# Optimization experiments

Measured on AMD Instinct MI355X. Metric: run time of the kernel, lower is better.

Reference implementation:

```python
import jax, jax.numpy as jnp
import numpy as np

N = 8192
IN_FEAT = 256
OUT_FEAT = 128
SLOPE = 0.1
NEG_INF = -9e15


def setup_inputs() -> dict:
    key = jax.random.key(0)
    k_doc, k_Ww, k_Wb, k_aw, k_ab = jax.random.split(key, 5)
    doc = jax.random.normal(k_doc, (N, IN_FEAT), dtype=jnp.float32)
    # nn.Linear(inFeat, outFeat): weight [out, in], bias [out]
    W_w = jax.random.normal(k_Ww, (OUT_FEAT, IN_FEAT), dtype=jnp.float32) / np.sqrt(IN_FEAT)
    W_b = jax.random.normal(k_Wb, (OUT_FEAT,), dtype=jnp.float32) * 0.01
    # nn.Linear(2*outFeat, 1): weight [1, 2*out], bias [1]
    a_w = jax.random.normal(k_aw, (1, 2 * OUT_FEAT), dtype=jnp.float32) / np.sqrt(2 * OUT_FEAT)
    a_b = jax.random.normal(k_ab, (1,), dtype=jnp.float32) * 0.01
    return {"doc": doc, "W_w": W_w, "W_b": W_b, "a_w": a_w, "a_b": a_b, "selfLink": 0}


def reference(doc, W_w, W_b, a_w, a_b, selfLink):
    # h = W(doc)  -> [N, outFeat]
    h = doc @ W_w.T + W_b
    n = h.shape[0]
    # Original builds fch[i, j] = concat(h_i, h_j) -> [N, N, 2D] and applies
    # Linear(2D, 1). Algebraically: score[i,j] = h_i . a_src + h_j . a_dst + b,
    # where a_src/a_dst are the two halves of the weight. Same math, O(N*D) mem.
    a_src = a_w[0, :OUT_FEAT]   # [D]
    a_dst = a_w[0, OUT_FEAT:]   # [D]
    s_src = h @ a_src           # [N]
    s_dst = h @ a_dst           # [N]
    att = jax.nn.leaky_relu(s_src[:, None] + s_dst[None, :] + a_b[0], SLOPE)  # [N, N]
    if selfLink == 0:
        # adj = 1 - eye: mask self-edges
        diag = jnp.eye(n, dtype=bool)
        att = jnp.where(diag, NEG_INF, att)
    att = jax.nn.softmax(att, axis=1)
    h_out = jax.nn.leaky_relu(att @ h, SLOPE)  # [N, D]
    return (h_out, att)
```

## Files before the change

### kernel.cpp

```cpp
#include <hip/hip_runtime.h>
#include <math.h>

#define NROW 8192
#define IN_F 256
#define OUT_F 128
#define SLOPE 0.1f

__device__ __forceinline__ float lrelu(float x) { return x > 0.f ? x : SLOPE * x; }

__global__ __launch_bounds__(256) void k1_h(const float* __restrict__ doc,
                                            const float* __restrict__ Ww,
                                            const float* __restrict__ Wb,
                                            float* __restrict__ h) {
    __shared__ float4 sdoc[16][64];
    const int t = threadIdx.x;
    const int rowBase = blockIdx.x * 16;
    const float4* doc4 = (const float4*)(doc + (size_t)rowBase * IN_F);
    float4* sflat = &sdoc[0][0];
    for (int i = t; i < 16 * 64; i += 256) sflat[i] = doc4[i];
    __syncthreads();
    const int c = t & 127;
    const int rg = t >> 7;
    float acc[8];
#pragma unroll
    for (int r = 0; r < 8; ++r) acc[r] = 0.f;
    const float4* w4 = (const float4*)(Ww + (size_t)c * IN_F);
    for (int k = 0; k < 64; ++k) {
        const float4 w = w4[k];
#pragma unroll
        for (int r = 0; r < 8; ++r) {
            const float4 d = sdoc[2 * r + rg][k];
            acc[r] += d.x * w.x + d.y * w.y + d.z * w.z + d.w * w.w;
        }
    }
    const float b = Wb[c];
#pragma unroll
    for (int r = 0; r < 8; ++r)
        h[(size_t)(rowBase + 2 * r + rg) * OUT_F + c] = acc[r] + b;
}

__global__ __launch_bounds__(256) void k1b_sv(const float* __restrict__ h,
                                              const float* __restrict__ aw,
                                              float* __restrict__ s_src,
                                              float* __restrict__ s_dst) {
    const int wave = threadIdx.x >> 6, lane = threadIdx.x & 63;
    const int row = blockIdx.x * 4 + wave;
    const float2 hv = ((const float2*)(h + (size_t)row * OUT_F))[lane];
    const float2 as = ((const float2*)aw)[lane];
    const float2 ad = ((const float2*)(aw + OUT_F))[lane];
    float ps = hv.x * as.x + hv.y * as.y;
    float pd = hv.x * ad.x + hv.y * ad.y;
    for (int off = 32; off; off >>= 1) {
        ps += __shfl_down(ps, off);
        pd += __shfl_down(pd, off);
    }
    if (lane == 0) { s_src[row] = ps; s_dst[row] = pd; }
}

__global__ __launch_bounds__(256) void k2_top2(const float* __restrict__ sdst,
                                               float* __restrict__ red,
                                               float* __restrict__ E1,
                                               float* __restrict__ E2) {
    const int t = threadIdx.x;
    float m1 = -1e30f, m2 = -1e30f; int i1 = 0;
    for (int j = t; j < NROW; j += 256) {
        const float v = sdst[j];
        E1[j] = expf(v);
        E2[j] = expf(SLOPE * v);
        if (v > m1) { m2 = m1; m1 = v; i1 = j; }
        else if (v > m2) { m2 = v; }
    }
    __shared__ float sm1[256], sm2[256];
    __shared__ int si[256];
    sm1[t] = m1; sm2[t] = m2; si[t] = i1;
    __syncthreads();
    for (int s = 128; s > 0; s >>= 1) {
        if (t < s) {
            const float om1 = sm1[t + s], om2 = sm2[t + s];
            const int oi = si[t + s];
            if (om1 > sm1[t]) {
                sm2[t] = fmaxf(sm1[t], om2);
                sm1[t] = om1; si[t] = oi;
            } else {
                sm2[t] = fmaxf(sm2[t], om1);
            }
        }
        __syncthreads();
    }
    if (t == 0) { red[0] = sm1[0]; red[1] = sm2[0]; red[2] = __int_as_float(si[0]); }
}

__global__ __launch_bounds__(256) void k2b_rank(const float* __restrict__ sdst,
                                                int* __restrict__ perm) {
    __shared__ float sd[NROW];
    for (int j = threadIdx.x; j < NROW; j += 256) sd[j] = sdst[j];
    __syncthreads();
    const int wave = threadIdx.x >> 6, lane = threadIdx.x & 63;
    const int i = blockIdx.x * 4 + wave;
    const float si_v = sd[i];
    int cnt = 0;
    for (int j = lane; j < NROW; j += 64) {
        const float v = sd[j];
        cnt += (v < si_v || (v == si_v && j < i)) ? 1 : 0;
    }
    for (int off = 32; off; off >>= 1) cnt += __shfl_down(cnt, off);
    if (lane == 0) perm[cnt] = i;
}

__global__ __launch_bounds__(256) void k3a_gather(const int* __restrict__ perm,
                                                  const float* __restrict__ E1,
                                                  const float* __restrict__ E2,
                                                  const float* __restrict__ sdst,
                                                  const float* __restrict__ h,
                                                  float* __restrict__ X1,
                                                  float* __restrict__ X2,
                                                  float* __restrict__ sortedS,
                                                  float* __restrict__ E1s,
                                                  float* __restrict__ E2s) {
    const int t = threadIdx.x;
    const int c = t & 127;
    const int half = t >> 7;
    const int base = blockIdx.x * 128;
    for (int rr = 0; rr < 64; ++rr) {
        const int r = base + rr * 2 + half;
        const int i = perm[r];
        const float hv = h[(size_t)i * OUT_F + c];
        X1[(size_t)r * OUT_F + c] = E1[i] * hv;
        X2[(size_t)r * OUT_F + c] = E2[i] * hv;
        if (c == 0) {
            sortedS[r] = sdst[i];
            E1s[r] = E1[i];
            E2s[r] = E2[i];
        }
    }
}

__global__ __launch_bounds__(256) void k3b1_segsum(const float* __restrict__ X1,
                                                   const float* __restrict__ X2,
                                                   float* __restrict__ seg1,
                                                   float* __restrict__ seg2) {
    const int tid = blockIdx.x * 256 + threadIdx.x;
    const int s = tid >> 7, c = tid & 127;
    float a = 0.f, b = 0.f;
    const int r0 = s * 128;
    for (int r = r0; r < r0 + 128; ++r) {
        a += X1[(size_t)r * OUT_F + c];
        b += X2[(size_t)r * OUT_F + c];
    }
    seg1[s * OUT_F + c] = a;
    seg2[s * OUT_F + c] = b;
}

__global__ __launch_bounds__(256) void k3b2_scan(const float* __restrict__ X1,
                                                 const float* __restrict__ X2,
                                                 const float* __restrict__ seg1,
                                                 const float* __restrict__ seg2,
                                                 float* __restrict__ U,
                                                 float* __restrict__ V) {
    const int tid = blockIdx.x * 256 + threadIdx.x;
    const int s = tid >> 7, c = tid & 127;
    float offU = 0.f, offV = 0.f;
    for (int s2 = s + 1; s2 < 64; ++s2) offU += seg1[s2 * OUT_F + c];
    for (int s2 = 0; s2 < s; ++s2) offV += seg2[s2 * OUT_F + c];
    const int r0 = s * 128;
    float run = offU;
    for (int r = r0 + 127; r >= r0; --r) {
        run += X1[(size_t)r * OUT_F + c];
        U[(size_t)r * OUT_F + c] = run;
    }
    float rv = offV;
    for (int r = r0; r < r0 + 128; ++r) {
        V[(size_t)r * OUT_F + c] = rv;
        rv += X2[(size_t)r * OUT_F + c];
    }
    if (s == 0) U[(size_t)NROW * OUT_F + c] = 0.f;
    if (s == 63) V[(size_t)NROW * OUT_F + c] = rv;
}

__global__ __launch_bounds__(256) void k3c_scalar(const float* __restrict__ E1s,
                                                  const float* __restrict__ E2s,
                                                  float* __restrict__ Psuf,
                                                  float* __restrict__ Qpre) {
    __shared__ float p1[256], p2[256];
    const int t = threadIdx.x;
    const int r0 = t * 32;
    float a = 0.f, b = 0.f;
    for (int r = r0; r < r0 + 32; ++r) { a += E1s[r]; b += E2s[r]; }
    p1[t] = a; p2[t] = b;
    __syncthreads();
    float offP = 0.f, offQ = 0.f;
    for (int t2 = t + 1; t2 < 256; ++t2) offP += p1[t2];
    for (int t2 = 0; t2 < t; ++t2) offQ += p2[t2];
    float run = offP;
    for (int r = r0 + 31; r >= r0; --r) { run += E1s[r]; Psuf[r] = run; }
    float rq = offQ;
    for (int r = r0; r < r0 + 32; ++r) { Qpre[r] = rq; rq += E2s[r]; }
    if (t == 0) Psuf[NROW] = 0.f;
    if (t == 255) Qpre[NROW] = rq;
}

__global__ __launch_bounds__(256) void k4pre(const float* __restrict__ s_src,
                                             const float* __restrict__ sdst,
                                             const float* __restrict__ sortedS,
                                             const float* __restrict__ Psuf,
                                             const float* __restrict__ Qpre,
                                             const float* __restrict__ red,
                                             const float* __restrict__ ab,
                                             const int* __restrict__ selfLink,
                                             float* __restrict__ A,
                                             float* __restrict__ B,
                                             float* __restrict__ rZ,
                                             float* __restrict__ Eii,
                                             float* __restrict__ Tarr,
                                             int* __restrict__ kidx) {
    const int i = blockIdx.x * 256 + threadIdx.x;
    const bool mask = (selfLink[0] == 0);
    const float t = s_src[i] + ab[0];
    const float M1 = red[0], M2 = red[1];
    const int i1 = __float_as_int(red[2]);
    const float M = (mask && i1 == i) ? M2 : M1;
    const float m = lrelu(t + M);
    const float Ai = expf(t - m);
    const float Bi = expf(SLOPE * t - m);
    const float eii = mask ? expf(lrelu(t + sdst[i]) - m) : 0.f;
    const float thr = -t;
    int lo = 0, hi = NROW;
    while (lo < hi) {
        const int mid = (lo + hi) >> 1;
        if (sortedS[mid] > thr) hi = mid; else lo = mid + 1;
    }
    const int k = lo;
    const float Z = Ai * Psuf[k] + Bi * Qpre[k] - eii;
    A[i] = Ai; B[i] = Bi; rZ[i] = 1.f / Z; Eii[i] = eii; Tarr[i] = t; kidx[i] = k;
}

__global__ __launch_bounds__(256) void k4a_hout(const float* __restrict__ A,
                                                const float* __restrict__ B,
                                                const float* __restrict__ rZ,
                                                const float* __restrict__ Eii,
                                                const int* __restrict__ kidx,
                                                const float* __restrict__ U,
                                                const float* __restrict__ V,
                                                const float* __restrict__ h,
                                                float* __restrict__ hout) {
    const int t = threadIdx.x;
    const int i = blockIdx.x * 2 + (t >> 7);
    const int c = t & 127;
    const int k = kidx[i];
    const float val = A[i] * U[(size_t)k * OUT_F + c] + B[i] * V[(size_t)k * OUT_F + c]
                    - Eii[i] * h[(size_t)i * OUT_F + c];
    hout[(size_t)i * OUT_F + c] = lrelu(val * rZ[i]);
}

#define ROWS5 8
#define JCH 2048
__global__ __launch_bounds__(256) void k5_att(const float* __restrict__ sdst,
                                              const float* __restrict__ E1,
                                              const float* __restrict__ E2,
                                              const float* __restrict__ A,
                                              const float* __restrict__ B,
                                              const float* __restrict__ rZ,
                                              const float* __restrict__ Tarr,
                                              const int* __restrict__ selfLink,
                                              float* __restrict__ att) {
    __shared__ float4 sS[JCH / 4], sE1[JCH / 4], sE2[JCH / 4];
    __shared__ float rA[ROWS5], rB[ROWS5], rT[ROWS5];
    const int t = threadIdx.x;
    const int rowBase = blockIdx.x * ROWS5;
    const bool mask = (selfLink[0] == 0);
    if (t < ROWS5) {
        const int i = rowBase + t;
        const float z = rZ[i];
        rA[t] = A[i] * z;
        rB[t] = B[i] * z;
        rT[t] = -Tarr[i];
    }
    for (int ch = 0; ch < NROW; ch += JCH) {
        __syncthreads();
        for (int q = t; q < JCH / 4; q += 256) {
            sS[q]  = ((const float4*)(sdst + ch))[q];
            sE1[q] = ((const float4*)(E1 + ch))[q];
            sE2[q] = ((const float4*)(E2 + ch))[q];
        }
        __syncthreads();
        for (int r = 0; r < ROWS5; ++r) {
            const int i = rowBase + r;
            const float a = rA[r], b = rB[r], thr = rT[r];
            for (int q = t; q < JCH / 4; q += 256) {
                const float4 s4 = sS[q], e1 = sE1[q], e2 = sE2[q];
                float4 o;
                o.x = s4.x > thr ? a * e1.x : b * e2.x;
                o.y = s4.y > thr ? a * e1.y : b * e2.y;
                o.z = s4.z > thr ? a * e1.z : b * e2.z;
                o.w = s4.w > thr ? a * e1.w : b * e2.w;
                const int j0 = ch + q * 4;
                if (mask && i >= j0 && i < j0 + 4) ((float*)&o)[i - j0] = 0.f;
                ((float4*)(att + (size_t)i * NROW + ch))[q] = o;
            }
        }
    }
}

extern "C" void kernel_launch(void* const* d_in, const int* in_sizes, int n_in,
                              void* d_out, int out_size, void* d_ws, size_t ws_size,
                              hipStream_t stream) {
    const float* doc = (const float*)d_in[0];
    const float* Ww  = (const float*)d_in[1];
    const float* Wb  = (const float*)d_in[2];
    const float* aw  = (const float*)d_in[3];
    const float* ab  = (const float*)d_in[4];
    const int* selfLink = (const int*)d_in[5];

    float* out  = (float*)d_out;
    float* hout = out;
    float* att  = out + (size_t)NROW * OUT_F;

    float* h  = att;
    float* X1 = att + 1048576;
    float* X2 = att + 2097152;
    float* U  = att + 3145728;
    float* V  = att + 4194432;

    float* ws = (float*)d_ws;
    float* s_src   = ws;
    float* s_dst   = ws + 8192;
    float* E1      = ws + 16384;
    float* E2      = ws + 24576;
    float* sortedS = ws + 32768;
    float* E1s     = ws + 40960;
    float* E2s     = ws + 49152;
    float* Aarr    = ws + 57344;
    float* Barr    = ws + 65536;
    float* rZ      = ws + 73728;
    float* Eii     = ws + 81920;
    float* Tarr    = ws + 90112;
    int*   perm    = (int*)(ws + 98304);
    int*   kidx    = (int*)(ws + 106496);
    float* seg1    = ws + 114688;
    float* seg2    = ws + 122880;
    float* Psuf    = ws + 131072;
    float* Qpre    = ws + 139272;
    float* red     = ws + 147472;

    k1_h   <<<512,  256, 0, stream>>>(doc, Ww, Wb, h);
    k1b_sv <<<2048, 256, 0, stream>>>(h, aw, s_src, s_dst);
    k2_top2<<<1,    256, 0, stream>>>(s_dst, red, E1, E2);
    k2b_rank<<<2048,256, 0, stream>>>(s_dst, perm);
    k3a_gather<<<64,256, 0, stream>>>(perm, E1, E2, s_dst, h, X1, X2, sortedS, E1s, E2s);
    k3b1_segsum<<<32,256,0, stream>>>(X1, X2, seg1, seg2);
    k3b2_scan<<<32, 256, 0, stream>>>(X1, X2, seg1, seg2, U, V);
    k3c_scalar<<<1, 256, 0, stream>>>(E1s, E2s, Psuf, Qpre);
    k4pre  <<<32,   256, 0, stream>>>(s_src, s_dst, sortedS, Psuf, Qpre, red, ab, selfLink,
                                      Aarr, Barr, rZ, Eii, Tarr, kidx);
    k4a_hout<<<4096,256, 0, stream>>>(Aarr, Barr, rZ, Eii, kidx, U, V, h, hout);
    k5_att <<<1024, 256, 0, stream>>>(s_dst, E1, E2, Aarr, Barr, rZ, Tarr, selfLink, att);
}
```

Baseline: 508.4 us.

## Fuse pipeline stages and restructure sorted-prefix scan into segment scan plus recompute

Fuses the score projection and exponentials into the linear-layer kernel, and rank computation now handles 8 rows per wave. The X1/X2 intermediates are no longer written. Segment sums are computed directly from gathered rows, scanned in parallel across 256 segments, and the U/V prefixes are rebuilt by re-gathering h. The per-row scalar precompute is folded into the h_out kernel. The aim is to cut kernel launches, global round-trips of large intermediates, and the serial long scans, at the cost of a second gather of h and redundant per-column scalar work in h_out.

```diff
diff --git a/kernel.cpp b/kernel.cpp
--- a/kernel.cpp
+++ b/kernel.cpp
@@ -5,14 +5,22 @@
 #define IN_F 256
 #define OUT_F 128
 #define SLOPE 0.1f
+#define SEGS 256
+#define SEGROWS 32
 
 __device__ __forceinline__ float lrelu(float x) { return x > 0.f ? x : SLOPE * x; }
 
-__global__ __launch_bounds__(256) void k1_h(const float* __restrict__ doc,
-                                            const float* __restrict__ Ww,
-                                            const float* __restrict__ Wb,
-                                            float* __restrict__ h) {
+__global__ __launch_bounds__(256) void kA_h_s(const float* __restrict__ doc,
+                                              const float* __restrict__ Ww,
+                                              const float* __restrict__ Wb,
+                                              const float* __restrict__ aw,
+                                              float* __restrict__ h,
+                                              float* __restrict__ s_src,
+                                              float* __restrict__ s_dst,
+                                              float* __restrict__ E1,
+                                              float* __restrict__ E2) {
     __shared__ float4 sdoc[16][64];
+    __shared__ float sred[4][8][2];
     const int t = threadIdx.x;
     const int rowBase = blockIdx.x * 16;
     const float4* doc4 = (const float4*)(doc + (size_t)rowBase * IN_F);
@@ -34,39 +42,46 @@
         }
     }
     const float b = Wb[c];
-#pragma unroll
-    for (int r = 0; r < 8; ++r)
-        h[(size_t)(rowBase + 2 * r + rg) * OUT_F + c] = acc[r] + b;
-}
-
-__global__ __launch_bounds__(256) void k1b_sv(const float* __restrict__ h,
-                                              const float* __restrict__ aw,
-                                              float* __restrict__ s_src,
-                                              float* __restrict__ s_dst) {
-    const int wave = threadIdx.x >> 6, lane = threadIdx.x & 63;
-    const int row = blockIdx.x * 4 + wave;
-    const float2 hv = ((const float2*)(h + (size_t)row * OUT_F))[lane];
-    const float2 as = ((const float2*)aw)[lane];
-    const float2 ad = ((const float2*)(aw + OUT_F))[lane];
-    float ps = hv.x * as.x + hv.y * as.y;
-    float pd = hv.x * ad.x + hv.y * ad.y;
-    for (int off = 32; off; off >>= 1) {
-        ps += __shfl_down(ps, off);
-        pd += __shfl_down(pd, off);
-    }
-    if (lane == 0) { s_src[row] = ps; s_dst[row] = pd; }
-}
-
-__global__ __launch_bounds__(256) void k2_top2(const float* __restrict__ sdst,
-                                               float* __restrict__ red,
-                                               float* __restrict__ E1,
-                                               float* __restrict__ E2) {
+    const float asrc = aw[c];
+    const float adst = aw[OUT_F + c];
+    const int wave = t >> 6;
+    const int lane = t & 63;
+#pragma unroll
+    for (int r = 0; r < 8; ++r) {
+        const float hv = acc[r] + b;
+        h[(size_t)(rowBase + 2 * r + rg) * OUT_F + c] = hv;
+        float ps = hv * asrc;
+        float pd = hv * adst;
+        for (int off = 32; off; off >>= 1) {
+            ps += __shfl_down(ps, off);
+            pd += __shfl_down(pd, off);
+        }
+        if (lane == 0) { sred[wave][r][0] = ps; sred[wave][r][1] = pd; }
+    }
+    __syncthreads();
+    if (t < 32) {
+        const int r = t >> 2;
+        const int rem = t & 3;
+        const int rg2 = rem >> 1;
+        const int which = rem & 1;
+        const float val = sred[2 * rg2][r][which] + sred[2 * rg2 + 1][r][which];
+        const int row = rowBase + 2 * r + rg2;
+        if (which == 0) {
+            s_src[row] = val;
+        } else {
+            s_dst[row] = val;
+            E1[row] = expf(val);
+            E2[row] = expf(SLOPE * val);
+        }
+    }
+}
+
+__global__ __launch_bounds__(256) void kB_top2(const float* __restrict__ sdst,
+                                               float* __restrict__ red) {
     const int t = threadIdx.x;
     float m1 = -1e30f, m2 = -1e30f; int i1 = 0;
     for (int j = t; j < NROW; j += 256) {
         const float v = sdst[j];
-        E1[j] = expf(v);
-        E2[j] = expf(SLOPE * v);
         if (v > m1) { m2 = m1; m1 = v; i1 = j; }
         else if (v > m2) { m2 = v; }
     }
@@ -90,140 +105,204 @@
     if (t == 0) { red[0] = sm1[0]; red[1] = sm2[0]; red[2] = __int_as_float(si[0]); }
 }
 
-__global__ __launch_bounds__(256) void k2b_rank(const float* __restrict__ sdst,
-                                                int* __restrict__ perm) {
+__global__ __launch_bounds__(256) void kC_rank(const float* __restrict__ sdst,
+                                               int* __restrict__ perm) {
     __shared__ float sd[NROW];
-    for (int j = threadIdx.x; j < NROW; j += 256) sd[j] = sdst[j];
+    {
+        float4* sd4 = (float4*)sd;
+        const float4* g4 = (const float4*)sdst;
+        for (int q = threadIdx.x; q < NROW / 4; q += 256) sd4[q] = g4[q];
+    }
     __syncthreads();
     const int wave = threadIdx.x >> 6, lane = threadIdx.x & 63;
-    const int i = blockIdx.x * 4 + wave;
-    const float si_v = sd[i];
-    int cnt = 0;
+    const int base = blockIdx.x * 32 + wave * 8;
+    float rv[8]; int ri[8]; int cnt[8];
+#pragma unroll
+    for (int r = 0; r < 8; ++r) { ri[r] = base + r; rv[r] = sd[ri[r]]; cnt[r] = 0; }
     for (int j = lane; j < NROW; j += 64) {
         const float v = sd[j];
-        cnt += (v < si_v || (v == si_v && j < i)) ? 1 : 0;
-    }
-    for (int off = 32; off; off >>= 1) cnt += __shfl_down(cnt, off);
-    if (lane == 0) perm[cnt] = i;
-}
-
-__global__ __launch_bounds__(256) void k3a_gather(const int* __restrict__ perm,
-                                                  const float* __restrict__ E1,
-                                                  const float* __restrict__ E2,
-                                                  const float* __restrict__ sdst,
-                                                  const float* __restrict__ h,
-                                                  float* __restrict__ X1,
-                                                  float* __restrict__ X2,
-                                                  float* __restrict__ sortedS,
-                                                  float* __restrict__ E1s,
-                                                  float* __restrict__ E2s) {
+#pragma unroll
+        for (int r = 0; r < 8; ++r)
+            cnt[r] += (v < rv[r] || (v == rv[r] && j < ri[r])) ? 1 : 0;
+    }
+#pragma unroll
+    for (int r = 0; r < 8; ++r)
+        for (int off = 32; off; off >>= 1) cnt[r] += __shfl_down(cnt[r], off);
+    if (lane == 0) {
+#pragma unroll
+        for (int r = 0; r < 8; ++r) perm[cnt[r]] = ri[r];
+    }
+}
+
+__global__ __launch_bounds__(256) void kD_gseg(const int* __restrict__ perm,
+                                               const float* __restrict__ E1,
+                                               const float* __restrict__ E2,
+                                               const float* __restrict__ sdst,
+                                               const float* __restrict__ h,
+                                               float* __restrict__ sortedS,
+                                               float* __restrict__ E1s,
+                                               float* __restrict__ E2s,
+                                               float* __restrict__ seg1,
+                                               float* __restrict__ seg2) {
+    __shared__ float part[2][4][128][2];
     const int t = threadIdx.x;
     const int c = t & 127;
     const int half = t >> 7;
     const int base = blockIdx.x * 128;
-    for (int rr = 0; rr < 64; ++rr) {
-        const int r = base + rr * 2 + half;
-        const int i = perm[r];
-        const float hv = h[(size_t)i * OUT_F + c];
-        X1[(size_t)r * OUT_F + c] = E1[i] * hv;
-        X2[(size_t)r * OUT_F + c] = E2[i] * hv;
-        if (c == 0) {
-            sortedS[r] = sdst[i];
-            E1s[r] = E1[i];
-            E2s[r] = E2[i];
-        }
-    }
-}
-
-__global__ __launch_bounds__(256) void k3b1_segsum(const float* __restrict__ X1,
-                                                   const float* __restrict__ X2,
-                                                   float* __restrict__ seg1,
-                                                   float* __restrict__ seg2) {
-    const int tid = blockIdx.x * 256 + threadIdx.x;
-    const int s = tid >> 7, c = tid & 127;
-    float a = 0.f, b = 0.f;
-    const int r0 = s * 128;
-    for (int r = r0; r < r0 + 128; ++r) {
-        a += X1[(size_t)r * OUT_F + c];
-        b += X2[(size_t)r * OUT_F + c];
-    }
-    seg1[s * OUT_F + c] = a;
-    seg2[s * OUT_F + c] = b;
-}
-
-__global__ __launch_bounds__(256) void k3b2_scan(const float* __restrict__ X1,
-                                                 const float* __restrict__ X2,
-                                                 const float* __restrict__ seg1,
-                                                 const float* __restrict__ seg2,
-                                                 float* __restrict__ U,
-                                                 float* __restrict__ V) {
-    const int tid = blockIdx.x * 256 + threadIdx.x;
-    const int s = tid >> 7, c = tid & 127;
-    float offU = 0.f, offV = 0.f;
-    for (int s2 = s + 1; s2 < 64; ++s2) offU += seg1[s2 * OUT_F + c];
-    for (int s2 = 0; s2 < s; ++s2) offV += seg2[s2 * OUT_F + c];
-    const int r0 = s * 128;
-    float run = offU;
-    for (int r = r0 + 127; r >= r0; --r) {
-        run += X1[(size_t)r * OUT_F + c];
-        U[(size_t)r * OUT_F + c] = run;
-    }
-    float rv = offV;
-    for (int r = r0; r < r0 + 128; ++r) {
-        V[(size_t)r * OUT_F + c] = rv;
-        rv += X2[(size_t)r * OUT_F + c];
-    }
-    if (s == 0) U[(size_t)NROW * OUT_F + c] = 0.f;
-    if (s == 63) V[(size_t)NROW * OUT_F + c] = rv;
-}
-
-__global__ __launch_bounds__(256) void k3c_scalar(const float* __restrict__ E1s,
-                                                  const float* __restrict__ E2s,
-                                                  float* __restrict__ Psuf,
-                                                  float* __restrict__ Qpre) {
-    __shared__ float p1[256], p2[256];
-    const int t = threadIdx.x;
-    const int r0 = t * 32;
-    float a = 0.f, b = 0.f;
-    for (int r = r0; r < r0 + 32; ++r) { a += E1s[r]; b += E2s[r]; }
-    p1[t] = a; p2[t] = b;
+    float a1[4] = {0.f, 0.f, 0.f, 0.f};
+    float a2[4] = {0.f, 0.f, 0.f, 0.f};
+#pragma unroll
+    for (int s = 0; s < 4; ++s) {
+        for (int rr2 = 0; rr2 < 16; ++rr2) {
+            const int rr = s * 16 + rr2;
+            const int lr = rr * 2 + half;
+            const int r = base + lr;
+            const int i = perm[r];
+            const float hv = h[(size_t)i * OUT_F + c];
+            const float e1 = E1[i];
+            const float e2 = E2[i];
+            a1[s] += e1 * hv;
+            a2[s] += e2 * hv;
+            if (c == 0) { sortedS[r] = sdst[i]; E1s[r] = e1; E2s[r] = e2; }
+        }
+        part[half][s][c][0] = a1[s];
+        part[half][s][c][1] = a2[s];
+    }
     __syncthreads();
-    float offP = 0.f, offQ = 0.f;
-    for (int t2 = t + 1; t2 < 256; ++t2) offP += p1[t2];
-    for (int t2 = 0; t2 < t; ++t2) offQ += p2[t2];
-    float run = offP;
-    for (int r = r0 + 31; r >= r0; --r) { run += E1s[r]; Psuf[r] = run; }
-    float rq = offQ;
-    for (int r = r0; r < r0 + 32; ++r) { Qpre[r] = rq; rq += E2s[r]; }
-    if (t == 0) Psuf[NROW] = 0.f;
-    if (t == 255) Qpre[NROW] = rq;
-}
-
-__global__ __launch_bounds__(256) void k4pre(const float* __restrict__ s_src,
-                                             const float* __restrict__ sdst,
-                                             const float* __restrict__ sortedS,
-                                             const float* __restrict__ Psuf,
-                                             const float* __restrict__ Qpre,
-                                             const float* __restrict__ red,
-                                             const float* __restrict__ ab,
-                                             const int* __restrict__ selfLink,
-                                             float* __restrict__ A,
-                                             float* __restrict__ B,
-                                             float* __restrict__ rZ,
-                                             float* __restrict__ Eii,
-                                             float* __restrict__ Tarr,
-                                             int* __restrict__ kidx) {
-    const int i = blockIdx.x * 256 + threadIdx.x;
+    const int idx4 = t * 4;
+#pragma unroll
+    for (int q = 0; q < 4; ++q) {
+        const int idx = idx4 + q;
+        const int arr = idx & 1;
+        const int c2 = (idx >> 1) & 127;
+        const int s2 = idx >> 8;
+        const float v = part[0][s2][c2][arr] + part[1][s2][c2][arr];
+        float* dst = arr ? seg2 : seg1;
+        dst[(size_t)(blockIdx.x * 4 + s2) * OUT_F + c2] = v;
+    }
+}
+
+__global__ __launch_bounds__(256) void kE_scan(const float* __restrict__ seg1,
+                                               const float* __restrict__ seg2,
+                                               const float* __restrict__ E1s,
+                                               const float* __restrict__ E2s,
+                                               float* __restrict__ segUo,
+                                               float* __restrict__ segVo,
+                                               float* __restrict__ Psuf,
+                                               float* __restrict__ Qpre) {
+    const int p = blockIdx.x;
+    const int t = threadIdx.x;
+    if (p < 256) {
+        const int arr = p >> 7;
+        const int col = p & 127;
+        const float* src = arr ? seg2 : seg1;
+        const float x = src[(size_t)t * OUT_F + col];
+        __shared__ float buf[256];
+        const int j = arr ? t : (255 - t);
+        buf[j] = x;
+        __syncthreads();
+        for (int off = 1; off < 256; off <<= 1) {
+            const float add = (j >= off) ? buf[j - off] : 0.f;
+            __syncthreads();
+            buf[j] += add;
+            __syncthreads();
+        }
+        const float excl = buf[j] - x;
+        float* dst = arr ? segVo : segUo;
+        dst[(size_t)t * OUT_F + col] = excl;
+    } else if (p == 256) {
+        __shared__ float pp[256];
+        const int r0 = t * 32;
+        float a = 0.f;
+        for (int rr = 0; rr < 32; ++rr) a += E1s[r0 + rr];
+        pp[t] = a;
+        __syncthreads();
+        float off = 0.f;
+        for (int t2 = t + 1; t2 < 256; ++t2) off += pp[t2];
+        float run = off;
+        for (int rr = 31; rr >= 0; --rr) { run += E1s[r0 + rr]; Psuf[r0 + rr] = run; }
+        if (t == 0) Psuf[NROW] = 0.f;
+    } else {
+        __shared__ float pp[256];
+        const int r0 = t * 32;
+        float a = 0.f;
+        for (int rr = 0; rr < 32; ++rr) a += E2s[r0 + rr];
+        pp[t] = a;
+        __syncthreads();
+        float off = 0.f;
+        for (int t2 = 0; t2 < t; ++t2) off += pp[t2];
+        float rv = off;
+        for (int rr = 0; rr < 32; ++rr) { Qpre[r0 + rr] = rv; rv += E2s[r0 + rr]; }
+        if (t == 255) Qpre[NROW] = rv;
+    }
+}
+
+__global__ __launch_bounds__(256) void kF_uv(const int* __restrict__ perm,
+                                             const float* __restrict__ h,
+                                             const float* __restrict__ E1s,
+                                             const float* __restrict__ E2s,
+                                             const float* __restrict__ segUo,
+                                             const float* __restrict__ segVo,
+                                             float* __restrict__ U,
+                                             float* __restrict__ V) {
+    const int t = threadIdx.x;
+    const int half = t >> 7;
+    const int c = t & 127;
+    const int s = blockIdx.x * 2 + half;
+    const int r0 = s * SEGROWS;
+    float xv[SEGROWS];
+#pragma unroll
+    for (int rr = 0; rr < SEGROWS; ++rr) {
+        const int i = perm[r0 + rr];
+        xv[rr] = h[(size_t)i * OUT_F + c];
+    }
+    float run = segUo[(size_t)s * OUT_F + c];
+#pragma unroll
+    for (int rr = SEGROWS - 1; rr >= 0; --rr) {
+        run += E1s[r0 + rr] * xv[rr];
+        U[(size_t)(r0 + rr) * OUT_F + c] = run;
+    }
+    float rv = segVo[(size_t)s * OUT_F + c];
+#pragma unroll
+    for (int rr = 0; rr < SEGROWS; ++rr) {
+        V[(size_t)(r0 + rr) * OUT_F + c] = rv;
+        rv += E2s[r0 + rr] * xv[rr];
+    }
+    if (s == SEGS - 1) {
+        U[(size_t)NROW * OUT_F + c] = 0.f;
+        V[(size_t)NROW * OUT_F + c] = rv;
+    }
+}
+
+__global__ __launch_bounds__(256) void kG_hout(const float* __restrict__ s_src,
+                                               const float* __restrict__ sdst,
+                                               const float* __restrict__ sortedS,
+                                               const float* __restrict__ Psuf,
+                                               const float* __restrict__ Qpre,
+                                               const float* __restrict__ red,
+                                               const float* __restrict__ ab,
+                                               const int* __restrict__ selfLink,
+                                               const float* __restrict__ U,
+                                               const float* __restrict__ V,
+                                               const float* __restrict__ h,
+                                               float* __restrict__ A,
+                                               float* __restrict__ B,
+                                               float* __restrict__ rZ,
+                                               float* __restrict__ T,
+                                               float* __restrict__ hout) {
+    const int t = threadIdx.x;
+    const int i = blockIdx.x * 2 + (t >> 7);
+    const int c = t & 127;
     const bool mask = (selfLink[0] == 0);
-    const float t = s_src[i] + ab[0];
+    const float tt = s_src[i] + ab[0];
     const float M1 = red[0], M2 = red[1];
     const int i1 = __float_as_int(red[2]);
     const float M = (mask && i1 == i) ? M2 : M1;
-    const float m = lrelu(t + M);
-    const float Ai = expf(t - m);
-    const float Bi = expf(SLOPE * t - m);
-    const float eii = mask ? expf(lrelu(t + sdst[i]) - m) : 0.f;
-    const float thr = -t;
+    const float m = lrelu(tt + M);
+    const float Ai = expf(tt - m);
+    const float Bi = expf(SLOPE * tt - m);
+    const float eii = mask ? expf(lrelu(tt + sdst[i]) - m) : 0.f;
+    const float thr = -tt;
     int lo = 0, hi = NROW;
     while (lo < hi) {
         const int mid = (lo + hi) >> 1;
@@ -231,36 +310,22 @@
     }
     const int k = lo;
     const float Z = Ai * Psuf[k] + Bi * Qpre[k] - eii;
-    A[i] = Ai; B[i] = Bi; rZ[i] = 1.f / Z; Eii[i] = eii; Tarr[i] = t; kidx[i] = k;
-}
-
-__global__ __launch_bounds__(256) void k4a_hout(const float* __restrict__ A,
-                                                const float* __restrict__ B,
-                                                const float* __restrict__ rZ,
-                                                const float* __restrict__ Eii,
-                                                const int* __restrict__ kidx,
-                                                const float* __restrict__ U,
-                                                const float* __restrict__ V,
-                                                const float* __restrict__ h,
-                                                float* __restrict__ hout) {
-    const int t = threadIdx.x;
-    const int i = blockIdx.x * 2 + (t >> 7);
-    const int c = t & 127;
-    const int k = kidx[i];
-    const float val = A[i] * U[(size_t)k * OUT_F + c] + B[i] * V[(size_t)k * OUT_F + c]
-                    - Eii[i] * h[(size_t)i * OUT_F + c];
-    hout[(size_t)i * OUT_F + c] = lrelu(val * rZ[i]);
+    const float rZi = 1.f / Z;
+    const float val = Ai * U[(size_t)k * OUT_F + c] + Bi * V[(size_t)k * OUT_F + c]
+                    - eii * h[(size_t)i * OUT_F + c];
+    hout[(size_t)i * OUT_F + c] = lrelu(val * rZi);
+    if (c == 0) { A[i] = Ai; B[i] = Bi; rZ[i] = rZi; T[i] = tt; }
 }
 
 #define ROWS5 8
 #define JCH 2048
-__global__ __launch_bounds__(256) void k5_att(const float* __restrict__ sdst,
+__global__ __launch_bounds__(256) void kH_att(const float* __restrict__ sdst,
                                               const float* __restrict__ E1,
                                               const float* __restrict__ E2,
                                               const float* __restrict__ A,
                                               const float* __restrict__ B,
                                               const float* __restrict__ rZ,
-                                              const float* __restrict__ Tarr,
+                                              const float* __restrict__ T,
                                               const int* __restrict__ selfLink,
                                               float* __restrict__ att) {
     __shared__ float4 sS[JCH / 4], sE1[JCH / 4], sE2[JCH / 4];
@@ -273,7 +338,7 @@
         const float z = rZ[i];
         rA[t] = A[i] * z;
         rB[t] = B[i] * z;
-        rT[t] = -Tarr[i];
+        rT[t] = -T[i];
     }
     for (int ch = 0; ch < NROW; ch += JCH) {
         __syncthreads();
@@ -315,11 +380,9 @@
     float* hout = out;
     float* att  = out + (size_t)NROW * OUT_F;
 
-    float* h  = att;
-    float* X1 = att + 1048576;
-    float* X2 = att + 2097152;
-    float* U  = att + 3145728;
-    float* V  = att + 4194432;
+    float* h = att;
+    float* U = att + 1048576;
+    float* V = att + 1048576 + 1048704;
 
     float* ws = (float*)d_ws;
     float* s_src   = ws;
@@ -332,26 +395,23 @@
     float* Aarr    = ws + 57344;
     float* Barr    = ws + 65536;
     float* rZ      = ws + 73728;
-    float* Eii     = ws + 81920;
-    float* Tarr    = ws + 90112;
-    int*   perm    = (int*)(ws + 98304);
-    int*   kidx    = (int*)(ws + 106496);
-    float* seg1    = ws + 114688;
-    float* seg2    = ws + 122880;
-    float* Psuf    = ws + 131072;
-    float* Qpre    = ws + 139272;
-    float* red     = ws + 147472;
-
-    k1_h   <<<512,  256, 0, stream>>>(doc, Ww, Wb, h);
-    k1b_sv <<<2048, 256, 0, stream>>>(h, aw, s_src, s_dst);
-    k2_top2<<<1,    256, 0, stream>>>(s_dst, red, E1, E2);
-    k2b_rank<<<2048,256, 0, stream>>>(s_dst, perm);
-    k3a_gather<<<64,256, 0, stream>>>(perm, E1, E2, s_dst, h, X1, X2, sortedS, E1s, E2s);
-    k3b1_segsum<<<32,256,0, stream>>>(X1, X2, seg1, seg2);
-    k3b2_scan<<<32, 256, 0, stream>>>(X1, X2, seg1, seg2, U, V);
-    k3c_scalar<<<1, 256, 0, stream>>>(E1s, E2s, Psuf, Qpre);
-    k4pre  <<<32,   256, 0, stream>>>(s_src, s_dst, sortedS, Psuf, Qpre, red, ab, selfLink,
-                                      Aarr, Barr, rZ, Eii, Tarr, kidx);
-    k4a_hout<<<4096,256, 0, stream>>>(Aarr, Barr, rZ, Eii, kidx, U, V, h, hout);
-    k5_att <<<1024, 256, 0, stream>>>(s_dst, E1, E2, Aarr, Barr, rZ, Tarr, selfLink, att);
-}
+    float* Tarr    = ws + 81920;
+    int*   perm    = (int*)(ws + 90112);
+    float* seg1    = ws + 98304;
+    float* seg2    = ws + 131072;
+    float* segUo   = ws + 163840;
+    float* segVo   = ws + 196608;
+    float* Psuf    = ws + 229376;
+    float* Qpre    = ws + 237632;
+    float* red     = ws + 245888;
+
+    kA_h_s <<<512,  256, 0, stream>>>(doc, Ww, Wb, aw, h, s_src, s_dst, E1, E2);
+    kB_top2<<<1,    256, 0, stream>>>(s_dst, red);
+    kC_rank<<<256,  256, 0, stream>>>(s_dst, perm);
+    kD_gseg<<<64,   256, 0, stream>>>(perm, E1, E2, s_dst, h, sortedS, E1s, E2s, seg1, seg2);
+    kE_scan<<<258,  256, 0, stream>>>(seg1, seg2, E1s, E2s, segUo, segVo, Psuf, Qpre);
+    kF_uv  <<<128,  256, 0, stream>>>(perm, h, E1s, E2s, segUo, segVo, U, V);
+    kG_hout<<<4096, 256, 0, stream>>>(s_src, s_dst, sortedS, Psuf, Qpre, red, ab, selfLink,
+                                      U, V, h, Aarr, Barr, rZ, Tarr, hout);
+    kH_att <<<1024, 256, 0, stream>>>(s_dst, E1, E2, Aarr, Barr, rZ, Tarr, selfLink, att);
+}
```

Measured after the change: 453.2 us. 1.12x faster.
